# Kernel tuning notes

Measured on AMD Instinct MI355X. Metric: run time of the kernel, lower is better.

Reference implementation:

```python
import jax, jax.numpy as jnp
import numpy as np


def _project_to_unitary_2x2(W):
    # Polar projection of batched 2x2 real matrices via SVD: U @ Vh.
    U, _, Vh = jnp.linalg.svd(W, full_matrices=False)
    return U @ Vh


def setup_inputs() -> dict:
    key = jax.random.key(0)
    k1, k2, k3 = jax.random.split(key, 3)
    B, T, C = 8, 4096, 2048
    G = C // 2
    x = jax.random.normal(k1, (B, T, C), dtype=jnp.float32)
    # Torch init: eye(2) + 0.01*randn per pair
    W_pairs = jnp.eye(2, dtype=jnp.float32)[None] + 0.01 * jax.random.normal(k2, (G, 2, 2), dtype=jnp.float32)
    phase = jax.random.normal(k3, (G,), dtype=jnp.float32)
    return {"x": x, "W_pairs": W_pairs, "phase": phase}


def reference(x, W_pairs, phase):
    B, T, C = x.shape
    G = C // 2
    # Project per-pair 2x2 to nearest orthonormal matrix (unitary_project=True)
    W = _project_to_unitary_2x2(W_pairs)  # [G,2,2]
    # Phase rotation matrices R(phi): [[c,-s],[s,c]]
    c, s = jnp.cos(phase), jnp.sin(phase)
    R = jnp.stack([jnp.stack([c, -s], -1), jnp.stack([s, c], -1)], -2)  # [G,2,2]
    # Compose rotation * unitary once, then apply as a single pass on [B,T,G,2]
    M = jnp.einsum('gij,gjk->gik', R, W)  # [G,2,2]
    xg = x.reshape(B, T, G, 2)
    y = jnp.einsum('gij,btgj->btgi', M, xg)
    return y.reshape(B, T, C)
```

## Files before the change

kernel.cpp:

```cpp
#include <hip/hip_runtime.h>

typedef float f32x4 __attribute__((ext_vector_type(4)));

__device__ __forceinline__ void compute_M(const float4* __restrict__ W,
                                          const float* __restrict__ phase,
                                          int g,
                                          float& m00, float& m01,
                                          float& m10, float& m11) {
    float4 w = W[g];
    float a = w.x, b = w.y, c = w.z, d = w.w;
    float det = a * d - b * c;
    float q00, q01, q10, q11;
    if (det >= 0.0f) {
        float p = a + d, q = b - c;
        float inv = rsqrtf(p * p + q * q);
        q00 = p * inv;  q01 = q * inv;
        q10 = -q * inv; q11 = p * inv;
    } else {
        float p = a - d, q = b + c;
        float inv = rsqrtf(p * p + q * q);
        q00 = p * inv; q01 = q * inv;
        q10 = q * inv; q11 = -p * inv;
    }
    float cs, sn;
    __sincosf(phase[g], &sn, &cs);
    m00 = cs * q00 - sn * q10;
    m01 = cs * q01 - sn * q11;
    m10 = sn * q00 + cs * q10;
    m11 = sn * q01 + cs * q11;
}

__global__ __launch_bounds__(256) void bsu_win(const f32x4* __restrict__ x,
                                               const float4* __restrict__ W,
                                               const float* __restrict__ phase,
                                               f32x4* __restrict__ y,
                                               int nwin, int gmask) {
    int t = threadIdx.x;
    int gA = (2 * t) & gmask;
    int gB = (2 * (t + 256)) & gmask;

    float a00, a01, a10, a11;
    float c00, c01, c10, c11;
    float e00, e01, e10, e11;
    float f00, f01, f10, f11;
    compute_M(W, phase, gA,     a00, a01, a10, a11);
    compute_M(W, phase, gA + 1, c00, c01, c10, c11);
    compute_M(W, phase, gB,     e00, e01, e10, e11);
    compute_M(W, phase, gB + 1, f00, f01, f10, f11);

    for (int w = blockIdx.x; w < nwin; w += gridDim.x) {
        int base = w * 1024 + t;
        f32x4 v0 = x[base];
        f32x4 v1 = x[base + 256];
        f32x4 v2 = x[base + 512];
        f32x4 v3 = x[base + 768];
        f32x4 o0, o1, o2, o3;
        o0.x = a00 * v0.x + a01 * v0.y;  o0.y = a10 * v0.x + a11 * v0.y;
        o0.z = c00 * v0.z + c01 * v0.w;  o0.w = c10 * v0.z + c11 * v0.w;
        o1.x = e00 * v1.x + e01 * v1.y;  o1.y = e10 * v1.x + e11 * v1.y;
        o1.z = f00 * v1.z + f01 * v1.w;  o1.w = f10 * v1.z + f11 * v1.w;
        o2.x = a00 * v2.x + a01 * v2.y;  o2.y = a10 * v2.x + a11 * v2.y;
        o2.z = c00 * v2.z + c01 * v2.w;  o2.w = c10 * v2.z + c11 * v2.w;
        o3.x = e00 * v3.x + e01 * v3.y;  o3.y = e10 * v3.x + e11 * v3.y;
        o3.z = f00 * v3.z + f01 * v3.w;  o3.w = f10 * v3.z + f11 * v3.w;
        y[base]       = o0;
        y[base + 256] = o1;
        y[base + 512] = o2;
        y[base + 768] = o3;
    }
}

__global__ __launch_bounds__(256) void bsu_fused(const f32x4* __restrict__ x,
                                                 const float4* __restrict__ W,
                                                 const float* __restrict__ phase,
                                                 f32x4* __restrict__ y,
                                                 int n4, int gmask) {
    int i0 = blockIdx.x * 256 + threadIdx.x;
    int stride = gridDim.x * 256;
    int g0 = (2 * i0) & gmask;

    float a00, a01, a10, a11;
    float b00, b01, b10, b11;
    compute_M(W, phase, g0,     a00, a01, a10, a11);
    compute_M(W, phase, g0 + 1, b00, b01, b10, b11);

    for (int i = i0; i < n4; i += stride) {
        f32x4 v = x[i];
        f32x4 o;
        o.x = a00 * v.x + a01 * v.y;
        o.y = a10 * v.x + a11 * v.y;
        o.z = b00 * v.z + b01 * v.w;
        o.w = b10 * v.z + b11 * v.w;
        y[i] = o;
    }
}

extern "C" void kernel_launch(void* const* d_in, const int* in_sizes, int n_in,
                              void* d_out, int out_size, void* d_ws, size_t ws_size,
                              hipStream_t stream) {
    const float* x     = (const float*)d_in[0];
    const float* Wp    = (const float*)d_in[1];
    const float* phase = (const float*)d_in[2];
    float* y = (float*)d_out;

    int G = in_sizes[2];
    int n = in_sizes[0];
    int n4 = n / 4;
    int row4 = G / 2;

    bool pow2G = (G & (G - 1)) == 0;
    if (pow2G && row4 > 0 && (1024 % row4) == 0 && (n4 % 1024) == 0) {
        int nwin = n4 / 1024;
        bsu_win<<<2048, 256, 0, stream>>>((const f32x4*)x, (const float4*)Wp,
                                          phase, (f32x4*)y, nwin, G - 1);
    } else {
        int blocks = 2048;
        if (!pow2G || (blocks * 256) % row4 != 0) blocks = (n4 + 255) / 256;
        bsu_fused<<<blocks, 256, 0, stream>>>((const f32x4*)x,
                                              (const float4*)Wp, phase,
                                              (f32x4*)y, n4, G - 1);
    }
}
```

Before: 101.1 us.

## Software-pipeline window loop with two-deep prefetch and nontemporal loads/stores

The grid-stride window loop becomes a software pipeline that keeps two future windows of loads in flight while the current window is computed and stored. All global loads and stores of x and y switch to nontemporal builtins so this streaming data bypasses or deprioritizes the cache. The aim is more memory-level parallelism per thread and less cache pollution on a purely bandwidth-bound kernel. In exchange it holds more live vector registers per thread, which may lower occupancy.

Measured after the change: 92.03 us. 9.0% less time.

```diff
diff --git a/kernel.cpp b/kernel.cpp
--- a/kernel.cpp
+++ b/kernel.cpp
@@ -30,11 +30,34 @@
     m11 = sn * q01 + cs * q11;
 }
 
-__global__ __launch_bounds__(256) void bsu_win(const f32x4* __restrict__ x,
-                                               const float4* __restrict__ W,
-                                               const float* __restrict__ phase,
-                                               f32x4* __restrict__ y,
-                                               int nwin, int gmask) {
+#define LOADW(dst0, dst1, dst2, dst3, base)                      \
+    dst0 = __builtin_nontemporal_load(&x[(base)]);               \
+    dst1 = __builtin_nontemporal_load(&x[(base) + 256]);         \
+    dst2 = __builtin_nontemporal_load(&x[(base) + 512]);         \
+    dst3 = __builtin_nontemporal_load(&x[(base) + 768]);
+
+#define APPLYSTORE(v0, v1, v2, v3, base)                                   \
+    {                                                                      \
+        f32x4 o0, o1, o2, o3;                                              \
+        o0.x = a00 * v0.x + a01 * v0.y;  o0.y = a10 * v0.x + a11 * v0.y;   \
+        o0.z = c00 * v0.z + c01 * v0.w;  o0.w = c10 * v0.z + c11 * v0.w;   \
+        o1.x = e00 * v1.x + e01 * v1.y;  o1.y = e10 * v1.x + e11 * v1.y;   \
+        o1.z = f00 * v1.z + f01 * v1.w;  o1.w = f10 * v1.z + f11 * v1.w;   \
+        o2.x = a00 * v2.x + a01 * v2.y;  o2.y = a10 * v2.x + a11 * v2.y;   \
+        o2.z = c00 * v2.z + c01 * v2.w;  o2.w = c10 * v2.z + c11 * v2.w;   \
+        o3.x = e00 * v3.x + e01 * v3.y;  o3.y = e10 * v3.x + e11 * v3.y;   \
+        o3.z = f00 * v3.z + f01 * v3.w;  o3.w = f10 * v3.z + f11 * v3.w;   \
+        __builtin_nontemporal_store(o0, &y[(base)]);                       \
+        __builtin_nontemporal_store(o1, &y[(base) + 256]);                 \
+        __builtin_nontemporal_store(o2, &y[(base) + 512]);                 \
+        __builtin_nontemporal_store(o3, &y[(base) + 768]);                 \
+    }
+
+__global__ __launch_bounds__(256) void bsu_win2(const f32x4* __restrict__ x,
+                                                const float4* __restrict__ W,
+                                                const float* __restrict__ phase,
+                                                f32x4* __restrict__ y,
+                                                int nwin, int gmask) {
     int t = threadIdx.x;
     int gA = (2 * t) & gmask;
     int gB = (2 * (t + 256)) & gmask;
@@ -48,25 +71,42 @@
     compute_M(W, phase, gB,     e00, e01, e10, e11);
     compute_M(W, phase, gB + 1, f00, f01, f10, f11);
 
-    for (int w = blockIdx.x; w < nwin; w += gridDim.x) {
-        int base = w * 1024 + t;
-        f32x4 v0 = x[base];
-        f32x4 v1 = x[base + 256];
-        f32x4 v2 = x[base + 512];
-        f32x4 v3 = x[base + 768];
-        f32x4 o0, o1, o2, o3;
-        o0.x = a00 * v0.x + a01 * v0.y;  o0.y = a10 * v0.x + a11 * v0.y;
-        o0.z = c00 * v0.z + c01 * v0.w;  o0.w = c10 * v0.z + c11 * v0.w;
-        o1.x = e00 * v1.x + e01 * v1.y;  o1.y = e10 * v1.x + e11 * v1.y;
-        o1.z = f00 * v1.z + f01 * v1.w;  o1.w = f10 * v1.z + f11 * v1.w;
-        o2.x = a00 * v2.x + a01 * v2.y;  o2.y = a10 * v2.x + a11 * v2.y;
-        o2.z = c00 * v2.z + c01 * v2.w;  o2.w = c10 * v2.z + c11 * v2.w;
-        o3.x = e00 * v3.x + e01 * v3.y;  o3.y = e10 * v3.x + e11 * v3.y;
-        o3.z = f00 * v3.z + f01 * v3.w;  o3.w = f10 * v3.z + f11 * v3.w;
-        y[base]       = o0;
-        y[base + 256] = o1;
-        y[base + 512] = o2;
-        y[base + 768] = o3;
+    int s = gridDim.x;
+    int wA = blockIdx.x;
+    if (wA >= nwin) return;
+
+    int baseA = wA * 1024 + t;
+    f32x4 A0, A1, A2, A3;
+    LOADW(A0, A1, A2, A3, baseA);
+
+    int wB = wA + s;
+    bool hasB = (wB < nwin);
+    int baseB = wB * 1024 + t;
+    f32x4 B0, B1, B2, B3;
+    if (hasB) { LOADW(B0, B1, B2, B3, baseB); }
+
+    while (true) {
+        int wC = wA + 2 * s;
+        bool hasC = (wC < nwin);
+        int baseC = wC * 1024 + t;
+        f32x4 C0, C1, C2, C3;
+        if (hasC) { LOADW(C0, C1, C2, C3, baseC); }
+
+        APPLYSTORE(A0, A1, A2, A3, baseA);
+        if (!hasB) break;
+
+        int wD = wB + 2 * s;
+        bool hasD = (wD < nwin);
+        int baseD = wD * 1024 + t;
+        f32x4 D0, D1, D2, D3;
+        if (hasD) { LOADW(D0, D1, D2, D3, baseD); }
+
+        APPLYSTORE(B0, B1, B2, B3, baseB);
+        if (!hasC) break;
+
+        A0 = C0; A1 = C1; A2 = C2; A3 = C3; baseA = baseC; wA = wC;
+        B0 = D0; B1 = D1; B2 = D2; B3 = D3; baseB = baseD; wB = wD;
+        hasB = hasD;
     }
 }
 
@@ -85,13 +125,13 @@
     compute_M(W, phase, g0 + 1, b00, b01, b10, b11);
 
     for (int i = i0; i < n4; i += stride) {
-        f32x4 v = x[i];
+        f32x4 v = __builtin_nontemporal_load(&x[i]);
         f32x4 o;
         o.x = a00 * v.x + a01 * v.y;
         o.y = a10 * v.x + a11 * v.y;
         o.z = b00 * v.z + b01 * v.w;
         o.w = b10 * v.z + b11 * v.w;
-        y[i] = o;
+        __builtin_nontemporal_store(o, &y[i]);
     }
 }
 
@@ -111,8 +151,8 @@
     bool pow2G = (G & (G - 1)) == 0;
     if (pow2G && row4 > 0 && (1024 % row4) == 0 && (n4 % 1024) == 0) {
         int nwin = n4 / 1024;
-        bsu_win<<<2048, 256, 0, stream>>>((const f32x4*)x, (const float4*)Wp,
-                                          phase, (f32x4*)y, nwin, G - 1);
+        bsu_win2<<<2048, 256, 0, stream>>>((const f32x4*)x, (const float4*)Wp,
+                                           phase, (f32x4*)y, nwin, G - 1);
     } else {
         int blocks = 2048;
         if (!pow2G || (blocks * 256) % row4 != 0) blocks = (n4 + 255) / 256;
```
